# Kernel tuning notes

Hardware: AMD Instinct MI355X
Metric: run time of the kernel (lower is better)

## Reference

```python
import jax, jax.numpy as jnp
import numpy as np

N_NODES = 50000
N_EDGES = 800000
F_IN = 256
HID = 128
HEADS = 4
F_OUT = 64
NEG_SLOPE = 0.2


def setup_inputs() -> dict:
    key = jax.random.key(0)
    ks = jax.random.split(key, 12)
    x = jax.random.normal(ks[0], (N_NODES, F_IN), dtype=jnp.float32)
    edge_index = jax.random.randint(ks[1], (2, N_EDGES), 0, N_NODES, dtype=jnp.int64)
    s = 0.05
    return {
        "x": x,
        "edge_index": edge_index,
        "W1": jax.random.normal(ks[2], (F_IN, HEADS * HID), dtype=jnp.float32) * s,
        "a_src1": jax.random.normal(ks[3], (HEADS, HID), dtype=jnp.float32) * s,
        "a_dst1": jax.random.normal(ks[4], (HEADS, HID), dtype=jnp.float32) * s,
        "b1": jnp.zeros((HEADS * HID,), dtype=jnp.float32),
        "W2": jax.random.normal(ks[5], (HEADS * HID, F_OUT), dtype=jnp.float32) * s,
        "a_src2": jax.random.normal(ks[6], (1, F_OUT), dtype=jnp.float32) * s,
        "a_dst2": jax.random.normal(ks[7], (1, F_OUT), dtype=jnp.float32) * s,
        "b2": jnp.zeros((F_OUT,), dtype=jnp.float32),
    }


def _add_self_loops(edge_index, n):
    loop = jnp.arange(n, dtype=edge_index.dtype)
    return jnp.concatenate([edge_index, jnp.stack([loop, loop])], axis=1)


def _gat_conv(x, edge_index, W, a_src, a_dst, bias, heads, out_ch):
    # PyG GATConv: h = x @ W reshaped to [N, H, C]
    n = x.shape[0]
    h = (x @ W).reshape(n, heads, out_ch)
    # per-node attention logits [N, H]
    al_src = jnp.einsum('nhc,hc->nh', h, a_src)
    al_dst = jnp.einsum('nhc,hc->nh', h, a_dst)
    src, dst = edge_index[0], edge_index[1]
    e = jax.nn.leaky_relu(al_src[src] + al_dst[dst], NEG_SLOPE)  # [E, H]
    # softmax over incoming edges per destination node (segment softmax)
    e_max = jax.ops.segment_max(e, dst, num_segments=n)
    e_exp = jnp.exp(e - e_max[dst])
    denom = jax.ops.segment_sum(e_exp, dst, num_segments=n)
    alpha = e_exp / (denom[dst] + 1e-16)  # [E, H]
    msg = h[src] * alpha[:, :, None]  # [E, H, C]
    out = jax.ops.segment_sum(msg, dst, num_segments=n)  # [N, H, C]
    return out.reshape(n, heads * out_ch) + bias


def reference(x, edge_index, W1, a_src1, a_dst1, b1, W2, a_src2, a_dst2, b2):
    # Dropout layers are identity in eval mode.
    ei = _add_self_loops(edge_index, x.shape[0])
    h = jax.nn.elu(_gat_conv(x, ei, W1, a_src1, a_dst1, b1, HEADS, HID))
    out = _gat_conv(h, ei, W2, a_src2, a_dst2, b2, 1, F_OUT)
    return out
```

## Files before the change

### kernel.cpp

```cpp
#include <hip/hip_runtime.h>
#include <math.h>

#define N_NODES 50000
#define N_EDGES 800000
#define E_TOT   850000
#define F_IN    256
#define F1      512
#define HID     128
#define HEADS   4
#define F_OUT   64

typedef __attribute__((ext_vector_type(8))) short short8;
typedef __attribute__((ext_vector_type(4))) float f32x4;
typedef unsigned short ushort_t;
typedef unsigned int uint_t;

__device__ __forceinline__ float lrelu(float x){ return x > 0.f ? x : 0.2f*x; }
__device__ __forceinline__ float elu(float x){ return x > 0.f ? x : expm1f(x); }

__device__ __forceinline__ ushort_t f2b(float f){
  uint_t u = __builtin_bit_cast(uint_t, f);
  u += 0x7fffu + ((u >> 16) & 1u);
  return (ushort_t)(u >> 16);
}
__device__ __forceinline__ float blo(uint_t u){ return __builtin_bit_cast(float, u << 16); }
__device__ __forceinline__ float bhi(uint_t u){ return __builtin_bit_cast(float, u & 0xffff0000u); }
__device__ __forceinline__ float b2f(ushort_t s){ return __builtin_bit_cast(float, (uint_t)s << 16); }

__global__ void hist_kernel(const int* __restrict__ ei, int* __restrict__ deg){
  int e = blockIdx.x*blockDim.x + threadIdx.x;
  if (e >= E_TOT) return;
  int dst = (e < N_EDGES) ? ei[N_EDGES + e] : (e - N_EDGES);
  atomicAdd(&deg[dst], 1);
}

__global__ __launch_bounds__(256) void scan1_kernel(const int* __restrict__ deg,
                                                    int* __restrict__ offs,
                                                    int* __restrict__ bsum){
  __shared__ int sd[256];
  const int tid = threadIdx.x;
  const int i = blockIdx.x*256 + tid;
  int v = (i < N_NODES) ? deg[i] : 0;
  sd[tid] = v; __syncthreads();
  #pragma unroll
  for (int off = 1; off < 256; off <<= 1){
    int t = (tid >= off) ? sd[tid - off] : 0;
    __syncthreads();
    sd[tid] += t;
    __syncthreads();
  }
  if (i < N_NODES) offs[i] = sd[tid] - v;
  if (tid == 255) bsum[blockIdx.x] = sd[255];
}

__global__ __launch_bounds__(256) void scan2_kernel(const int* __restrict__ bsum,
                                                    int* __restrict__ bbase, int nb){
  __shared__ int sd[256];
  const int tid = threadIdx.x;
  int v = (tid < nb) ? bsum[tid] : 0;
  sd[tid] = v; __syncthreads();
  #pragma unroll
  for (int off = 1; off < 256; off <<= 1){
    int t = (tid >= off) ? sd[tid - off] : 0;
    __syncthreads();
    sd[tid] += t;
    __syncthreads();
  }
  if (tid < nb) bbase[tid] = sd[tid] - v;
}

__global__ __launch_bounds__(256) void scan3_kernel(int* __restrict__ offs,
                                                    const int* __restrict__ bbase,
                                                    int* __restrict__ cur){
  const int i = blockIdx.x*256 + threadIdx.x;
  if (i < N_NODES){
    int o = offs[i] + bbase[blockIdx.x];
    offs[i] = o;
    cur[i] = o;
  }
  if (blockIdx.x == 0 && threadIdx.x == 0) offs[N_NODES] = E_TOT;
}

__global__ void scatter_kernel(const int* __restrict__ ei, int* __restrict__ cur,
                               int* __restrict__ ssrc){
  int e = blockIdx.x*blockDim.x + threadIdx.x;
  if (e >= E_TOT) return;
  int src, dst;
  if (e < N_EDGES){ src = ei[e]; dst = ei[N_EDGES + e]; }
  else            { src = e - N_EDGES; dst = src; }
  int pos = atomicAdd(&cur[dst], 1);
  ssrc[pos] = src;
}

__global__ __launch_bounds__(256) void cvt_x_kernel(const float* __restrict__ x,
                                                    ushort_t* __restrict__ xb){
  const int t = blockIdx.x*256 + threadIdx.x;
  const float4 a = ((const float4*)x)[t*2];
  const float4 b = ((const float4*)x)[t*2 + 1];
  uint4 o;
  o.x = (uint_t)f2b(a.x) | ((uint_t)f2b(a.y) << 16);
  o.y = (uint_t)f2b(a.z) | ((uint_t)f2b(a.w) << 16);
  o.z = (uint_t)f2b(b.x) | ((uint_t)f2b(b.y) << 16);
  o.w = (uint_t)f2b(b.z) | ((uint_t)f2b(b.w) << 16);
  ((uint4*)xb)[t] = o;
}

__global__ __launch_bounds__(256) void transpose_bf16_kernel(const float* __restrict__ W,
                                                             ushort_t* __restrict__ Wt,
                                                             int K, int N){
  __shared__ float tile[64][65];
  const int k0 = blockIdx.x*64, n0 = blockIdx.y*64;
  const int c = threadIdx.x & 63, r4 = threadIdx.x >> 6;
  for (int r = r4; r < 64; r += 4)
    tile[r][c] = W[(size_t)(k0 + r)*N + n0 + c];
  __syncthreads();
  for (int r = r4; r < 64; r += 4)
    Wt[(size_t)(n0 + r)*K + k0 + c] = f2b(tile[c][r]);
}

template<int K, int WR, int WC>
__global__ __launch_bounds__(256) void gemm_bf16(const ushort_t* __restrict__ A,
                                                 const ushort_t* __restrict__ Bt,
                                                 ushort_t* __restrict__ C,
                                                 int M, int N){
  constexpr int BM = WR*64, BN = WC*64, BKP = 40;
  __shared__ ushort_t As[BM*BKP];
  __shared__ ushort_t Bs[BN*BKP];
  const int tid = threadIdx.x;
  const int wave = tid >> 6, lane = tid & 63, quad = lane >> 4, l16 = lane & 15;
  const int wm = wave % WR, wn = wave / WR;
  const int m0 = blockIdx.x*BM, n0 = blockIdx.y*BN;
  f32x4 acc[4][4] = {};
  for (int k0 = 0; k0 < K; k0 += 32){
    #pragma unroll
    for (int s = tid; s < BM*4; s += 256){
      int r = s >> 2, c = s & 3;
      int gr = m0 + r; if (gr >= M) gr = M - 1;
      *(uint4*)(As + r*BKP + c*8) = *(const uint4*)(A + (size_t)gr*K + k0 + c*8);
    }
    #pragma unroll
    for (int s = tid; s < BN*4; s += 256){
      int r = s >> 2, c = s & 3;
      *(uint4*)(Bs + r*BKP + c*8) = *(const uint4*)(Bt + (size_t)(n0 + r)*K + k0 + c*8);
    }
    __syncthreads();
    short8 af[4], bfr[4];
    #pragma unroll
    for (int i = 0; i < 4; ++i)
      af[i] = *(const short8*)(As + (wm*64 + i*16 + l16)*BKP + quad*8);
    #pragma unroll
    for (int j = 0; j < 4; ++j)
      bfr[j] = *(const short8*)(Bs + (wn*64 + j*16 + l16)*BKP + quad*8);
    #pragma unroll
    for (int i = 0; i < 4; ++i)
      #pragma unroll
      for (int j = 0; j < 4; ++j)
        acc[i][j] = __builtin_amdgcn_mfma_f32_16x16x32_bf16(af[i], bfr[j], acc[i][j], 0, 0, 0);
    __syncthreads();
  }
  #pragma unroll
  for (int i = 0; i < 4; ++i){
    #pragma unroll
    for (int r = 0; r < 4; ++r){
      int row = m0 + wm*64 + i*16 + quad*4 + r;
      if (row < M){
        #pragma unroll
        for (int j = 0; j < 4; ++j){
          int col = n0 + wn*64 + j*16 + l16;
          C[(size_t)row*N + col] = f2b(acc[i][j][r]);
        }
      }
    }
  }
}

__global__ __launch_bounds__(128) void logits1_kernel(const ushort_t* __restrict__ h1b,
                                                      const float* __restrict__ a_src,
                                                      const float* __restrict__ a_dst,
                                                      float* __restrict__ als,
                                                      float* __restrict__ ald){
  const int n = blockIdx.x;
  const int tid = threadIdx.x;
  const int head = tid >> 5, p = tid & 31;
  const uint2 v = *(const uint2*)(h1b + (size_t)n*F1 + tid*4);
  float h0 = blo(v.x), h1 = bhi(v.x), h2 = blo(v.y), h3 = bhi(v.y);
  const float4 as = *(const float4*)(a_src + head*HID + p*4);
  const float4 ad = *(const float4*)(a_dst + head*HID + p*4);
  float ds = h0*as.x + h1*as.y + h2*as.z + h3*as.w;
  float dd = h0*ad.x + h1*ad.y + h2*ad.z + h3*ad.w;
  #pragma unroll
  for (int off = 16; off >= 1; off >>= 1){
    ds += __shfl_down(ds, off, 32);
    dd += __shfl_down(dd, off, 32);
  }
  if (p == 0){ als[n*4 + head] = ds; ald[n*4 + head] = dd; }
}

__global__ __launch_bounds__(256) void agg1_kernel(const ushort_t* __restrict__ h1b,
                                                   const float* __restrict__ als,
                                                   const float* __restrict__ ald1,
                                                   const float* __restrict__ b1,
                                                   const int* __restrict__ offs,
                                                   const int* __restrict__ ssrc,
                                                   ushort_t* __restrict__ hb){
  __shared__ int   shsrc[4][64];
  __shared__ float shal[4][64][4];
  const int wave = threadIdx.x >> 6, lane = threadIdx.x & 63;
  const int n = blockIdx.x*4 + wave;
  const int head = lane >> 4;
  const float4 ald = ((const float4*)ald1)[n];
  const int s0 = offs[n], s1 = offs[n+1];

  float d0 = 0.f, d1 = 0.f, d2 = 0.f, d3 = 0.f;
  for (int e = s0 + lane; e < s1; e += 64){
    const int sc = ssrc[e];
    const float4 as = ((const float4*)als)[sc];
    d0 += __expf(lrelu(as.x + ald.x));
    d1 += __expf(lrelu(as.y + ald.y));
    d2 += __expf(lrelu(as.z + ald.z));
    d3 += __expf(lrelu(as.w + ald.w));
  }
  #pragma unroll
  for (int off = 32; off >= 1; off >>= 1){
    d0 += __shfl_xor(d0, off);
    d1 += __shfl_xor(d1, off);
    d2 += __shfl_xor(d2, off);
    d3 += __shfl_xor(d3, off);
  }
  const float den = (head == 0) ? d0 : (head == 1) ? d1 : (head == 2) ? d2 : d3;
  const float rd = 1.0f / (den + 1e-16f);

  float acc[8] = {0.f,0.f,0.f,0.f,0.f,0.f,0.f,0.f};
  for (int ce = s0; ce < s1; ce += 64){
    const int idx = ce + lane;
    if (idx < s1){
      const int sc = ssrc[idx];
      const float4 as = ((const float4*)als)[sc];
      shsrc[wave][lane] = sc;
      float4 a4;
      a4.x = __expf(lrelu(as.x + ald.x));
      a4.y = __expf(lrelu(as.y + ald.y));
      a4.z = __expf(lrelu(as.z + ald.z));
      a4.w = __expf(lrelu(as.w + ald.w));
      *(float4*)&shal[wave][lane][0] = a4;
    }
    const int nE = min(64, s1 - ce);
    for (int k = 0; k < nE; ++k){
      const int scb = shsrc[wave][k];
      const float al = shal[wave][k][head] * rd;
      const uint4 hv = *(const uint4*)(h1b + (size_t)scb*F1 + lane*8);
      acc[0] = fmaf(blo(hv.x), al, acc[0]);
      acc[1] = fmaf(bhi(hv.x), al, acc[1]);
      acc[2] = fmaf(blo(hv.y), al, acc[2]);
      acc[3] = fmaf(bhi(hv.y), al, acc[3]);
      acc[4] = fmaf(blo(hv.z), al, acc[4]);
      acc[5] = fmaf(bhi(hv.z), al, acc[5]);
      acc[6] = fmaf(blo(hv.w), al, acc[6]);
      acc[7] = fmaf(bhi(hv.w), al, acc[7]);
    }
  }
  const float4 ba = *(const float4*)(b1 + lane*8);
  const float4 bb = *(const float4*)(b1 + lane*8 + 4);
  float o0 = elu(acc[0] + ba.x), o1 = elu(acc[1] + ba.y);
  float o2 = elu(acc[2] + ba.z), o3 = elu(acc[3] + ba.w);
  float o4 = elu(acc[4] + bb.x), o5 = elu(acc[5] + bb.y);
  float o6 = elu(acc[6] + bb.z), o7 = elu(acc[7] + bb.w);
  uint4 o;
  o.x = (uint_t)f2b(o0) | ((uint_t)f2b(o1) << 16);
  o.y = (uint_t)f2b(o2) | ((uint_t)f2b(o3) << 16);
  o.z = (uint_t)f2b(o4) | ((uint_t)f2b(o5) << 16);
  o.w = (uint_t)f2b(o6) | ((uint_t)f2b(o7) << 16);
  *(uint4*)(hb + (size_t)n*F1 + lane*8) = o;
}

__global__ __launch_bounds__(64) void logits2_kernel(const ushort_t* __restrict__ gb,
                                                     const float* __restrict__ a_src,
                                                     const float* __restrict__ a_dst,
                                                     float* __restrict__ als,
                                                     float* __restrict__ ald){
  const int n = blockIdx.x;
  const int tid = threadIdx.x;
  const float v = b2f(gb[(size_t)n*F_OUT + tid]);
  float ds = v * a_src[tid];
  float dd = v * a_dst[tid];
  #pragma unroll
  for (int off = 32; off >= 1; off >>= 1){
    ds += __shfl_xor(ds, off);
    dd += __shfl_xor(dd, off);
  }
  if (tid == 0){ als[n] = ds; ald[n] = dd; }
}

__global__ __launch_bounds__(256) void agg2_kernel(const ushort_t* __restrict__ gb,
                                                   const float* __restrict__ als,
                                                   const float* __restrict__ ald2,
                                                   const float* __restrict__ b2,
                                                   const int* __restrict__ offs,
                                                   const int* __restrict__ ssrc,
                                                   float* __restrict__ out){
  __shared__ int   shsrc[4][64];
  __shared__ float shal[4][64];
  const int wave = threadIdx.x >> 6, lane = threadIdx.x & 63;
  const int n = blockIdx.x*4 + wave;
  const float ald = ald2[n];
  const int s0 = offs[n], s1 = offs[n+1];

  float dsum = 0.f;
  for (int e = s0 + lane; e < s1; e += 64)
    dsum += __expf(lrelu(als[ssrc[e]] + ald));
  #pragma unroll
  for (int off = 32; off >= 1; off >>= 1)
    dsum += __shfl_xor(dsum, off);
  const float rd = 1.0f / (dsum + 1e-16f);

  float acc = 0.f;
  for (int ce = s0; ce < s1; ce += 64){
    const int idx = ce + lane;
    if (idx < s1){
      const int sc = ssrc[idx];
      shsrc[wave][lane] = sc;
      shal[wave][lane] = __expf(lrelu(als[sc] + ald)) * rd;
    }
    const int nE = min(64, s1 - ce);
    for (int k = 0; k < nE; ++k){
      const int scb = shsrc[wave][k];
      const float al = shal[wave][k];
      acc = fmaf(b2f(gb[(size_t)scb*F_OUT + lane]), al, acc);
    }
  }
  out[(size_t)n*F_OUT + lane] = acc + b2[lane];
}

extern "C" void kernel_launch(void* const* d_in, const int* in_sizes, int n_in,
                              void* d_out, int out_size, void* d_ws, size_t ws_size,
                              hipStream_t stream){
  const float* x      = (const float*)d_in[0];
  const int*   ei     = (const int*)  d_in[1];
  const float* W1     = (const float*)d_in[2];
  const float* a_src1 = (const float*)d_in[3];
  const float* a_dst1 = (const float*)d_in[4];
  const float* b1     = (const float*)d_in[5];
  const float* W2     = (const float*)d_in[6];
  const float* a_src2 = (const float*)d_in[7];
  const float* a_dst2 = (const float*)d_in[8];
  const float* b2     = (const float*)d_in[9];
  float* out = (float*)d_out;

  char* ws = (char*)d_ws;
  ushort_t* h1b  = (ushort_t*)(ws + 0UL);
  ushort_t* hb   = (ushort_t*)(ws + 51200000UL);
  ushort_t* xb   = (ushort_t*)(ws + 102400000UL);
  ushort_t* gb   = (ushort_t*)(ws + 128000000UL);
  ushort_t* W1t  = (ushort_t*)(ws + 134400000UL);
  ushort_t* W2t  = (ushort_t*)(ws + 134662144UL);
  float*    als1 = (float*)   (ws + 134727680UL);
  float*    ald1 = (float*)   (ws + 135527680UL);
  float*    als2 = (float*)   (ws + 136327680UL);
  float*    ald2 = (float*)   (ws + 136527680UL);
  int*      deg  = (int*)     (ws + 136727680UL);
  int*      offs = (int*)     (ws + 136927680UL);
  int*      bsum = (int*)     (ws + 137127744UL);
  int*      bbase= (int*)     (ws + 137128544UL);
  int*      cur  = (int*)     (ws + 137129600UL);
  int*      ssrc = (int*)     (ws + 137329600UL);

  hipMemsetAsync(deg, 0, 200000, stream);

  const int eb = (E_TOT + 255) / 256;
  const int nb = (N_NODES + 255) / 256;
  hist_kernel   <<<eb, 256, 0, stream>>>(ei, deg);
  scan1_kernel  <<<nb, 256, 0, stream>>>(deg, offs, bsum);
  scan2_kernel  <<<1, 256, 0, stream>>>(bsum, bbase, nb);
  scan3_kernel  <<<nb, 256, 0, stream>>>(offs, bbase, cur);
  scatter_kernel<<<eb, 256, 0, stream>>>(ei, cur, ssrc);

  cvt_x_kernel        <<<6250, 256, 0, stream>>>(x, xb);
  transpose_bf16_kernel<<<dim3(4, 8), 256, 0, stream>>>(W1, W1t, F_IN, F1);
  transpose_bf16_kernel<<<dim3(8, 1), 256, 0, stream>>>(W2, W2t, F1, F_OUT);

  gemm_bf16<F_IN, 2, 2><<<dim3(391, 4), 256, 0, stream>>>(xb, W1t, h1b, N_NODES, F1);
  logits1_kernel<<<N_NODES, 128, 0, stream>>>(h1b, a_src1, a_dst1, als1, ald1);
  agg1_kernel   <<<12500, 256, 0, stream>>>(h1b, als1, ald1, b1, offs, ssrc, hb);

  gemm_bf16<F1, 4, 1><<<dim3(196, 1), 256, 0, stream>>>(hb, W2t, gb, N_NODES, F_OUT);
  logits2_kernel<<<N_NODES, 64, 0, stream>>>(gb, a_src2, a_dst2, als2, ald2);
  agg2_kernel   <<<12500, 256, 0, stream>>>(gb, als2, ald2, b2, offs, ssrc, out);
}
```

Baseline: 469.2 us.

## Use split-bf16 GEMMs with fused logits, sorted CSR, and vectorized layer-2 aggregation

Replaces the single-bf16 GEMMs with a three-MFMA hi/lo split scheme for higher accuracy. Attention logits are now computed in the GEMM epilogue, which removes the two separate logits kernels. The change also adds a per-node sort of source indices, loads GEMM tiles with global_load_lds, pre-normalizes alphas in agg1, stores layer-2 features as fp32 and vectorizes agg2 so each load fetches four edges. The split precision triples the MFMA work and doubles operand traffic, and the new sort kernel adds work of its own.

```diff
diff --git a/kernel.cpp b/kernel.cpp
--- a/kernel.cpp
+++ b/kernel.cpp
@@ -26,6 +26,16 @@
 __device__ __forceinline__ float blo(uint_t u){ return __builtin_bit_cast(float, u << 16); }
 __device__ __forceinline__ float bhi(uint_t u){ return __builtin_bit_cast(float, u & 0xffff0000u); }
 __device__ __forceinline__ float b2f(ushort_t s){ return __builtin_bit_cast(float, (uint_t)s << 16); }
+
+__device__ __forceinline__ void fsplit(float v, ushort_t& hi, ushort_t& lo){
+  hi = f2b(v);
+  lo = f2b(v - b2f(hi));
+}
+
+__device__ __forceinline__ void gld_lds16(const void* g, void* l){
+  __builtin_amdgcn_global_load_lds((const __attribute__((address_space(1))) unsigned int*)g,
+                                   (__attribute__((address_space(3))) unsigned int*)l, 16, 0, 0);
+}
 
 __global__ void hist_kernel(const int* __restrict__ ei, int* __restrict__ deg){
   int e = blockIdx.x*blockDim.x + threadIdx.x;
@@ -92,70 +102,127 @@
   ssrc[pos] = src;
 }
 
-__global__ __launch_bounds__(256) void cvt_x_kernel(const float* __restrict__ x,
-                                                    ushort_t* __restrict__ xb){
+__global__ __launch_bounds__(256) void sort_kernel(const int* __restrict__ offs,
+                                                   int* __restrict__ ssrc){
+  const int wave = threadIdx.x >> 6, lane = threadIdx.x & 63;
+  const int n = blockIdx.x*4 + wave;
+  const int s0 = offs[n];
+  const int len = offs[n+1] - s0;
+  if (len <= 1) return;
+  if (len <= 64){
+    int v = (lane < len) ? ssrc[s0 + lane] : 0x7fffffff;
+    for (int p = 0; p < len; ++p){
+      const int left = ((lane & 1) == (p & 1));
+      const int partner = left ? lane + 1 : lane - 1;
+      const int pv = __shfl(v, partner & 63);
+      const int nv = left ? min(v, pv) : max(v, pv);
+      v = (partner >= 0 && partner < 64) ? nv : v;
+    }
+    if (lane < len) ssrc[s0 + lane] = v;
+  } else if (lane == 0){
+    for (int i = 1; i < len; ++i){
+      int v = ssrc[s0 + i]; int j = i - 1;
+      while (j >= 0 && ssrc[s0 + j] > v){ ssrc[s0 + j + 1] = ssrc[s0 + j]; --j; }
+      ssrc[s0 + j + 1] = v;
+    }
+  }
+}
+
+__global__ __launch_bounds__(256) void cvt_x_split_kernel(const float* __restrict__ x,
+                                                          ushort_t* __restrict__ xh,
+                                                          ushort_t* __restrict__ xl){
   const int t = blockIdx.x*256 + threadIdx.x;
   const float4 a = ((const float4*)x)[t*2];
   const float4 b = ((const float4*)x)[t*2 + 1];
-  uint4 o;
-  o.x = (uint_t)f2b(a.x) | ((uint_t)f2b(a.y) << 16);
-  o.y = (uint_t)f2b(a.z) | ((uint_t)f2b(a.w) << 16);
-  o.z = (uint_t)f2b(b.x) | ((uint_t)f2b(b.y) << 16);
-  o.w = (uint_t)f2b(b.z) | ((uint_t)f2b(b.w) << 16);
-  ((uint4*)xb)[t] = o;
-}
-
-__global__ __launch_bounds__(256) void transpose_bf16_kernel(const float* __restrict__ W,
-                                                             ushort_t* __restrict__ Wt,
-                                                             int K, int N){
+  float v[8] = {a.x,a.y,a.z,a.w,b.x,b.y,b.z,b.w};
+  ushort_t h[8], l[8];
+  #pragma unroll
+  for (int i = 0; i < 8; ++i) fsplit(v[i], h[i], l[i]);
+  uint4 oh, ol;
+  oh.x = (uint_t)h[0] | ((uint_t)h[1] << 16);
+  oh.y = (uint_t)h[2] | ((uint_t)h[3] << 16);
+  oh.z = (uint_t)h[4] | ((uint_t)h[5] << 16);
+  oh.w = (uint_t)h[6] | ((uint_t)h[7] << 16);
+  ol.x = (uint_t)l[0] | ((uint_t)l[1] << 16);
+  ol.y = (uint_t)l[2] | ((uint_t)l[3] << 16);
+  ol.z = (uint_t)l[4] | ((uint_t)l[5] << 16);
+  ol.w = (uint_t)l[6] | ((uint_t)l[7] << 16);
+  ((uint4*)xh)[t] = oh;
+  ((uint4*)xl)[t] = ol;
+}
+
+__global__ __launch_bounds__(256) void transpose_split_kernel(const float* __restrict__ W,
+                                                              ushort_t* __restrict__ Wth,
+                                                              ushort_t* __restrict__ Wtl,
+                                                              int K, int N){
   __shared__ float tile[64][65];
   const int k0 = blockIdx.x*64, n0 = blockIdx.y*64;
   const int c = threadIdx.x & 63, r4 = threadIdx.x >> 6;
   for (int r = r4; r < 64; r += 4)
     tile[r][c] = W[(size_t)(k0 + r)*N + n0 + c];
   __syncthreads();
-  for (int r = r4; r < 64; r += 4)
-    Wt[(size_t)(n0 + r)*K + k0 + c] = f2b(tile[c][r]);
-}
-
-template<int K, int WR, int WC>
-__global__ __launch_bounds__(256) void gemm_bf16(const ushort_t* __restrict__ A,
-                                                 const ushort_t* __restrict__ Bt,
-                                                 ushort_t* __restrict__ C,
-                                                 int M, int N){
-  constexpr int BM = WR*64, BN = WC*64, BKP = 40;
-  __shared__ ushort_t As[BM*BKP];
-  __shared__ ushort_t Bs[BN*BKP];
+  for (int r = r4; r < 64; r += 4){
+    ushort_t hi, lo;
+    fsplit(tile[c][r], hi, lo);
+    Wth[(size_t)(n0 + r)*K + k0 + c] = hi;
+    Wtl[(size_t)(n0 + r)*K + k0 + c] = lo;
+  }
+}
+
+template<int K, int BM, int BN, int WR, int WC, int NH, int CH, bool CF32>
+__global__ __launch_bounds__(256) void gemm_x3(const ushort_t* __restrict__ Ah,
+                                               const ushort_t* __restrict__ Al,
+                                               const ushort_t* __restrict__ Bh,
+                                               const ushort_t* __restrict__ Bl,
+                                               void* __restrict__ Cout,
+                                               const float* __restrict__ a_src,
+                                               const float* __restrict__ a_dst,
+                                               float* __restrict__ als,
+                                               float* __restrict__ ald,
+                                               int M){
+  constexpr int NTOT = NH*CH;
+  __shared__ ushort_t Ash[BM*32], Asl[BM*32];
+  __shared__ ushort_t Bsh[BN*32], Bsl[BN*32];
+  __shared__ float slog[WC][BM][2];
   const int tid = threadIdx.x;
   const int wave = tid >> 6, lane = tid & 63, quad = lane >> 4, l16 = lane & 15;
   const int wm = wave % WR, wn = wave / WR;
-  const int m0 = blockIdx.x*BM, n0 = blockIdx.y*BN;
+  const int m0 = blockIdx.x*BM;
+  const int head = blockIdx.y;
+  const int n0 = head*BN;
   f32x4 acc[4][4] = {};
   for (int k0 = 0; k0 < K; k0 += 32){
+    for (int idx = tid; idx < BM*4; idx += 256){
+      int row = idx >> 2, ch = idx & 3;
+      int gr = m0 + row; gr = (gr < M) ? gr : (M - 1);
+      gld_lds16(Ah + (size_t)gr*K + k0 + ch*8, (char*)Ash + idx*16);
+      gld_lds16(Al + (size_t)gr*K + k0 + ch*8, (char*)Asl + idx*16);
+    }
+    for (int idx = tid; idx < BN*4; idx += 256){
+      int row = idx >> 2, ch = idx & 3;
+      gld_lds16(Bh + (size_t)(n0 + row)*K + k0 + ch*8, (char*)Bsh + idx*16);
+      gld_lds16(Bl + (size_t)(n0 + row)*K + k0 + ch*8, (char*)Bsl + idx*16);
+    }
+    __syncthreads();
+    short8 afh[4], afl[4], bfh[4], bfl[4];
     #pragma unroll
-    for (int s = tid; s < BM*4; s += 256){
-      int r = s >> 2, c = s & 3;
-      int gr = m0 + r; if (gr >= M) gr = M - 1;
-      *(uint4*)(As + r*BKP + c*8) = *(const uint4*)(A + (size_t)gr*K + k0 + c*8);
+    for (int i = 0; i < 4; ++i){
+      afh[i] = *(const short8*)(Ash + (wm*64 + i*16 + l16)*32 + quad*8);
+      afl[i] = *(const short8*)(Asl + (wm*64 + i*16 + l16)*32 + quad*8);
     }
     #pragma unroll
-    for (int s = tid; s < BN*4; s += 256){
-      int r = s >> 2, c = s & 3;
-      *(uint4*)(Bs + r*BKP + c*8) = *(const uint4*)(Bt + (size_t)(n0 + r)*K + k0 + c*8);
-    }
-    __syncthreads();
-    short8 af[4], bfr[4];
-    #pragma unroll
-    for (int i = 0; i < 4; ++i)
-      af[i] = *(const short8*)(As + (wm*64 + i*16 + l16)*BKP + quad*8);
-    #pragma unroll
-    for (int j = 0; j < 4; ++j)
-      bfr[j] = *(const short8*)(Bs + (wn*64 + j*16 + l16)*BKP + quad*8);
+    for (int j = 0; j < 4; ++j){
+      bfh[j] = *(const short8*)(Bsh + (wn*64 + j*16 + l16)*32 + quad*8);
+      bfl[j] = *(const short8*)(Bsl + (wn*64 + j*16 + l16)*32 + quad*8);
+    }
     #pragma unroll
     for (int i = 0; i < 4; ++i)
       #pragma unroll
-      for (int j = 0; j < 4; ++j)
-        acc[i][j] = __builtin_amdgcn_mfma_f32_16x16x32_bf16(af[i], bfr[j], acc[i][j], 0, 0, 0);
+      for (int j = 0; j < 4; ++j){
+        acc[i][j] = __builtin_amdgcn_mfma_f32_16x16x32_bf16(afh[i], bfh[j], acc[i][j], 0, 0, 0);
+        acc[i][j] = __builtin_amdgcn_mfma_f32_16x16x32_bf16(afl[i], bfh[j], acc[i][j], 0, 0, 0);
+        acc[i][j] = __builtin_amdgcn_mfma_f32_16x16x32_bf16(afh[i], bfl[j], acc[i][j], 0, 0, 0);
+      }
     __syncthreads();
   }
   #pragma unroll
@@ -167,33 +234,48 @@
         #pragma unroll
         for (int j = 0; j < 4; ++j){
           int col = n0 + wn*64 + j*16 + l16;
-          C[(size_t)row*N + col] = f2b(acc[i][j][r]);
+          if (CF32) ((float*)Cout)[(size_t)row*NTOT + col] = acc[i][j][r];
+          else      ((ushort_t*)Cout)[(size_t)row*NTOT + col] = f2b(acc[i][j][r]);
         }
       }
     }
   }
-}
-
-__global__ __launch_bounds__(128) void logits1_kernel(const ushort_t* __restrict__ h1b,
-                                                      const float* __restrict__ a_src,
-                                                      const float* __restrict__ a_dst,
-                                                      float* __restrict__ als,
-                                                      float* __restrict__ ald){
-  const int n = blockIdx.x;
-  const int tid = threadIdx.x;
-  const int head = tid >> 5, p = tid & 31;
-  const uint2 v = *(const uint2*)(h1b + (size_t)n*F1 + tid*4);
-  float h0 = blo(v.x), h1 = bhi(v.x), h2 = blo(v.y), h3 = bhi(v.y);
-  const float4 as = *(const float4*)(a_src + head*HID + p*4);
-  const float4 ad = *(const float4*)(a_dst + head*HID + p*4);
-  float ds = h0*as.x + h1*as.y + h2*as.z + h3*as.w;
-  float dd = h0*ad.x + h1*ad.y + h2*ad.z + h3*ad.w;
-  #pragma unroll
-  for (int off = 16; off >= 1; off >>= 1){
-    ds += __shfl_down(ds, off, 32);
-    dd += __shfl_down(dd, off, 32);
-  }
-  if (p == 0){ als[n*4 + head] = ds; ald[n*4 + head] = dd; }
+  float aws[4], awd[4];
+  #pragma unroll
+  for (int j = 0; j < 4; ++j){
+    int cih = wn*64 + j*16 + l16;
+    aws[j] = a_src[head*CH + cih];
+    awd[j] = a_dst[head*CH + cih];
+  }
+  #pragma unroll
+  for (int i = 0; i < 4; ++i){
+    #pragma unroll
+    for (int r = 0; r < 4; ++r){
+      float s = acc[i][0][r]*aws[0] + acc[i][1][r]*aws[1]
+              + acc[i][2][r]*aws[2] + acc[i][3][r]*aws[3];
+      float d = acc[i][0][r]*awd[0] + acc[i][1][r]*awd[1]
+              + acc[i][2][r]*awd[2] + acc[i][3][r]*awd[3];
+      #pragma unroll
+      for (int off = 8; off >= 1; off >>= 1){
+        s += __shfl_xor(s, off);
+        d += __shfl_xor(d, off);
+      }
+      if (l16 == 0){
+        slog[wn][wm*64 + i*16 + quad*4 + r][0] = s;
+        slog[wn][wm*64 + i*16 + quad*4 + r][1] = d;
+      }
+    }
+  }
+  __syncthreads();
+  for (int t = tid; t < BM; t += 256){
+    float s = slog[0][t][0], d = slog[0][t][1];
+    if (WC > 1){ s += slog[WC-1][t][0]; d += slog[WC-1][t][1]; }
+    int row = m0 + t;
+    if (row < M){
+      als[row*NH + head] = s;
+      ald[row*NH + head] = d;
+    }
+  }
 }
 
 __global__ __launch_bounds__(256) void agg1_kernel(const ushort_t* __restrict__ h1b,
@@ -202,7 +284,8 @@
                                                    const float* __restrict__ b1,
                                                    const int* __restrict__ offs,
                                                    const int* __restrict__ ssrc,
-                                                   ushort_t* __restrict__ hb){
+                                                   ushort_t* __restrict__ hbh,
+                                                   ushort_t* __restrict__ hbl){
   __shared__ int   shsrc[4][64];
   __shared__ float shal[4][64][4];
   const int wave = threadIdx.x >> 6, lane = threadIdx.x & 63;
@@ -227,8 +310,8 @@
     d2 += __shfl_xor(d2, off);
     d3 += __shfl_xor(d3, off);
   }
-  const float den = (head == 0) ? d0 : (head == 1) ? d1 : (head == 2) ? d2 : d3;
-  const float rd = 1.0f / (den + 1e-16f);
+  const float rd0 = 1.0f/(d0 + 1e-16f), rd1 = 1.0f/(d1 + 1e-16f);
+  const float rd2 = 1.0f/(d2 + 1e-16f), rd3 = 1.0f/(d3 + 1e-16f);
 
   float acc[8] = {0.f,0.f,0.f,0.f,0.f,0.f,0.f,0.f};
   for (int ce = s0; ce < s1; ce += 64){
@@ -238,60 +321,53 @@
       const float4 as = ((const float4*)als)[sc];
       shsrc[wave][lane] = sc;
       float4 a4;
-      a4.x = __expf(lrelu(as.x + ald.x));
-      a4.y = __expf(lrelu(as.y + ald.y));
-      a4.z = __expf(lrelu(as.z + ald.z));
-      a4.w = __expf(lrelu(as.w + ald.w));
+      a4.x = __expf(lrelu(as.x + ald.x)) * rd0;
+      a4.y = __expf(lrelu(as.y + ald.y)) * rd1;
+      a4.z = __expf(lrelu(as.z + ald.z)) * rd2;
+      a4.w = __expf(lrelu(as.w + ald.w)) * rd3;
       *(float4*)&shal[wave][lane][0] = a4;
     }
+    __builtin_amdgcn_wave_barrier();
     const int nE = min(64, s1 - ce);
     for (int k = 0; k < nE; ++k){
-      const int scb = shsrc[wave][k];
-      const float al = shal[wave][k][head] * rd;
-      const uint4 hv = *(const uint4*)(h1b + (size_t)scb*F1 + lane*8);
-      acc[0] = fmaf(blo(hv.x), al, acc[0]);
-      acc[1] = fmaf(bhi(hv.x), al, acc[1]);
-      acc[2] = fmaf(blo(hv.y), al, acc[2]);
-      acc[3] = fmaf(bhi(hv.y), al, acc[3]);
-      acc[4] = fmaf(blo(hv.z), al, acc[4]);
-      acc[5] = fmaf(bhi(hv.z), al, acc[5]);
-      acc[6] = fmaf(blo(hv.w), al, acc[6]);
-      acc[7] = fmaf(bhi(hv.w), al, acc[7]);
-    }
+      const int sa = shsrc[wave][k];
+      const float aa = shal[wave][k][head];
+      const uint4 ha = *(const uint4*)(h1b + (size_t)sa*F1 + lane*8);
+      acc[0] = fmaf(blo(ha.x), aa, acc[0]);
+      acc[1] = fmaf(bhi(ha.x), aa, acc[1]);
+      acc[2] = fmaf(blo(ha.y), aa, acc[2]);
+      acc[3] = fmaf(bhi(ha.y), aa, acc[3]);
+      acc[4] = fmaf(blo(ha.z), aa, acc[4]);
+      acc[5] = fmaf(bhi(ha.z), aa, acc[5]);
+      acc[6] = fmaf(blo(ha.w), aa, acc[6]);
+      acc[7] = fmaf(bhi(ha.w), aa, acc[7]);
+    }
+    __builtin_amdgcn_wave_barrier();
   }
   const float4 ba = *(const float4*)(b1 + lane*8);
   const float4 bb = *(const float4*)(b1 + lane*8 + 4);
-  float o0 = elu(acc[0] + ba.x), o1 = elu(acc[1] + ba.y);
-  float o2 = elu(acc[2] + ba.z), o3 = elu(acc[3] + ba.w);
-  float o4 = elu(acc[4] + bb.x), o5 = elu(acc[5] + bb.y);
-  float o6 = elu(acc[6] + bb.z), o7 = elu(acc[7] + bb.w);
-  uint4 o;
-  o.x = (uint_t)f2b(o0) | ((uint_t)f2b(o1) << 16);
-  o.y = (uint_t)f2b(o2) | ((uint_t)f2b(o3) << 16);
-  o.z = (uint_t)f2b(o4) | ((uint_t)f2b(o5) << 16);
-  o.w = (uint_t)f2b(o6) | ((uint_t)f2b(o7) << 16);
-  *(uint4*)(hb + (size_t)n*F1 + lane*8) = o;
-}
-
-__global__ __launch_bounds__(64) void logits2_kernel(const ushort_t* __restrict__ gb,
-                                                     const float* __restrict__ a_src,
-                                                     const float* __restrict__ a_dst,
-                                                     float* __restrict__ als,
-                                                     float* __restrict__ ald){
-  const int n = blockIdx.x;
-  const int tid = threadIdx.x;
-  const float v = b2f(gb[(size_t)n*F_OUT + tid]);
-  float ds = v * a_src[tid];
-  float dd = v * a_dst[tid];
-  #pragma unroll
-  for (int off = 32; off >= 1; off >>= 1){
-    ds += __shfl_xor(ds, off);
-    dd += __shfl_xor(dd, off);
-  }
-  if (tid == 0){ als[n] = ds; ald[n] = dd; }
-}
-
-__global__ __launch_bounds__(256) void agg2_kernel(const ushort_t* __restrict__ gb,
+  float o[8];
+  o[0] = elu(acc[0] + ba.x); o[1] = elu(acc[1] + ba.y);
+  o[2] = elu(acc[2] + ba.z); o[3] = elu(acc[3] + ba.w);
+  o[4] = elu(acc[4] + bb.x); o[5] = elu(acc[5] + bb.y);
+  o[6] = elu(acc[6] + bb.z); o[7] = elu(acc[7] + bb.w);
+  ushort_t h[8], l[8];
+  #pragma unroll
+  for (int i = 0; i < 8; ++i) fsplit(o[i], h[i], l[i]);
+  uint4 oh, ol;
+  oh.x = (uint_t)h[0] | ((uint_t)h[1] << 16);
+  oh.y = (uint_t)h[2] | ((uint_t)h[3] << 16);
+  oh.z = (uint_t)h[4] | ((uint_t)h[5] << 16);
+  oh.w = (uint_t)h[6] | ((uint_t)h[7] << 16);
+  ol.x = (uint_t)l[0] | ((uint_t)l[1] << 16);
+  ol.y = (uint_t)l[2] | ((uint_t)l[3] << 16);
+  ol.z = (uint_t)l[4] | ((uint_t)l[5] << 16);
+  ol.w = (uint_t)l[6] | ((uint_t)l[7] << 16);
+  *(uint4*)(hbh + (size_t)n*F1 + lane*8) = oh;
+  *(uint4*)(hbl + (size_t)n*F1 + lane*8) = ol;
+}
+
+__global__ __launch_bounds__(256) void agg2_kernel(const float* __restrict__ gb,
                                                    const float* __restrict__ als,
                                                    const float* __restrict__ ald2,
                                                    const float* __restrict__ b2,
@@ -302,6 +378,7 @@
   __shared__ float shal[4][64];
   const int wave = threadIdx.x >> 6, lane = threadIdx.x & 63;
   const int n = blockIdx.x*4 + wave;
+  const int g = lane >> 4, l16 = lane & 15;
   const float ald = ald2[n];
   const int s0 = offs[n], s1 = offs[n+1];
 
@@ -313,7 +390,7 @@
     dsum += __shfl_xor(dsum, off);
   const float rd = 1.0f / (dsum + 1e-16f);
 
-  float acc = 0.f;
+  float a0 = 0.f, a1 = 0.f, a2 = 0.f, a3 = 0.f;
   for (int ce = s0; ce < s1; ce += 64){
     const int idx = ce + lane;
     if (idx < s1){
@@ -321,14 +398,30 @@
       shsrc[wave][lane] = sc;
       shal[wave][lane] = __expf(lrelu(als[sc] + ald)) * rd;
     }
+    __builtin_amdgcn_wave_barrier();
     const int nE = min(64, s1 - ce);
-    for (int k = 0; k < nE; ++k){
-      const int scb = shsrc[wave][k];
-      const float al = shal[wave][k];
-      acc = fmaf(b2f(gb[(size_t)scb*F_OUT + lane]), al, acc);
-    }
-  }
-  out[(size_t)n*F_OUT + lane] = acc + b2[lane];
+    for (int k = 0; k < nE; k += 4){
+      const int e = k + g;
+      float al = 0.f;
+      int sc = shsrc[wave][0];
+      if (e < nE){ sc = shsrc[wave][e]; al = shal[wave][e]; }
+      const float4 hv = *(const float4*)(gb + (size_t)sc*F_OUT + l16*4);
+      a0 = fmaf(hv.x, al, a0);
+      a1 = fmaf(hv.y, al, a1);
+      a2 = fmaf(hv.z, al, a2);
+      a3 = fmaf(hv.w, al, a3);
+    }
+    __builtin_amdgcn_wave_barrier();
+  }
+  a0 += __shfl_xor(a0, 16); a0 += __shfl_xor(a0, 32);
+  a1 += __shfl_xor(a1, 16); a1 += __shfl_xor(a1, 32);
+  a2 += __shfl_xor(a2, 16); a2 += __shfl_xor(a2, 32);
+  a3 += __shfl_xor(a3, 16); a3 += __shfl_xor(a3, 32);
+  if (g == 0){
+    const float4 bv = *(const float4*)(b2 + l16*4);
+    float4 o = {a0 + bv.x, a1 + bv.y, a2 + bv.z, a3 + bv.w};
+    *(float4*)(out + (size_t)n*F_OUT + l16*4) = o;
+  }
 }
 
 extern "C" void kernel_launch(void* const* d_in, const int* in_sizes, int n_in,
@@ -347,22 +440,26 @@
   float* out = (float*)d_out;
 
   char* ws = (char*)d_ws;
-  ushort_t* h1b  = (ushort_t*)(ws + 0UL);
-  ushort_t* hb   = (ushort_t*)(ws + 51200000UL);
-  ushort_t* xb   = (ushort_t*)(ws + 102400000UL);
-  ushort_t* gb   = (ushort_t*)(ws + 128000000UL);
-  ushort_t* W1t  = (ushort_t*)(ws + 134400000UL);
-  ushort_t* W2t  = (ushort_t*)(ws + 134662144UL);
-  float*    als1 = (float*)   (ws + 134727680UL);
-  float*    ald1 = (float*)   (ws + 135527680UL);
-  float*    als2 = (float*)   (ws + 136327680UL);
-  float*    ald2 = (float*)   (ws + 136527680UL);
-  int*      deg  = (int*)     (ws + 136727680UL);
-  int*      offs = (int*)     (ws + 136927680UL);
-  int*      bsum = (int*)     (ws + 137127744UL);
-  int*      bbase= (int*)     (ws + 137128544UL);
-  int*      cur  = (int*)     (ws + 137129600UL);
-  int*      ssrc = (int*)     (ws + 137329600UL);
+  ushort_t* xh   = (ushort_t*)(ws + 0UL);
+  ushort_t* xl   = (ushort_t*)(ws + 25600000UL);
+  ushort_t* hbh  = (ushort_t*)(ws + 0UL);
+  ushort_t* h1b  = (ushort_t*)(ws + 51200000UL);
+  ushort_t* hbl  = (ushort_t*)(ws + 102400000UL);
+  float*    gb   = (float*)   (ws + 153600000UL);
+  ushort_t* W1th = (ushort_t*)(ws + 166400000UL);
+  ushort_t* W1tl = (ushort_t*)(ws + 166662144UL);
+  ushort_t* W2th = (ushort_t*)(ws + 166924288UL);
+  ushort_t* W2tl = (ushort_t*)(ws + 166989824UL);
+  float*    als1 = (float*)   (ws + 167055360UL);
+  float*    ald1 = (float*)   (ws + 167855360UL);
+  float*    als2 = (float*)   (ws + 168655360UL);
+  float*    ald2 = (float*)   (ws + 168855360UL);
+  int*      deg  = (int*)     (ws + 169055360UL);
+  int*      offs = (int*)     (ws + 169255360UL);
+  int*      bsum = (int*)     (ws + 169455616UL);
+  int*      bbase= (int*)     (ws + 169456640UL);
+  int*      cur  = (int*)     (ws + 169457664UL);
+  int*      ssrc = (int*)     (ws + 169657664UL);
 
   hipMemsetAsync(deg, 0, 200000, stream);
 
@@ -373,16 +470,19 @@
   scan2_kernel  <<<1, 256, 0, stream>>>(bsum, bbase, nb);
   scan3_kernel  <<<nb, 256, 0, stream>>>(offs, bbase, cur);
   scatter_kernel<<<eb, 256, 0, stream>>>(ei, cur, ssrc);
-
-  cvt_x_kernel        <<<6250, 256, 0, stream>>>(x, xb);
-  transpose_bf16_kernel<<<dim3(4, 8), 256, 0, stream>>>(W1, W1t, F_IN, F1);
-  transpose_bf16_kernel<<<dim3(8, 1), 256, 0, stream>>>(W2, W2t, F1, F_OUT);
-
-  gemm_bf16<F_IN, 2, 2><<<dim3(391, 4), 256, 0, stream>>>(xb, W1t, h1b, N_NODES, F1);
-  logits1_kernel<<<N_NODES, 128, 0, stream>>>(h1b, a_src1, a_dst1, als1, ald1);
-  agg1_kernel   <<<12500, 256, 0, stream>>>(h1b, als1, ald1, b1, offs, ssrc, hb);
-
-  gemm_bf16<F1, 4, 1><<<dim3(196, 1), 256, 0, stream>>>(hb, W2t, gb, N_NODES, F_OUT);
-  logits2_kernel<<<N_NODES, 64, 0, stream>>>(gb, a_src2, a_dst2, als2, ald2);
-  agg2_kernel   <<<12500, 256, 0, stream>>>(gb, als2, ald2, b2, offs, ssrc, out);
-}
+  sort_kernel   <<<12500, 256, 0, stream>>>(offs, ssrc);
+
+  cvt_x_split_kernel   <<<6250, 256, 0, stream>>>(x, xh, xl);
+  transpose_split_kernel<<<dim3(4, 8), 256, 0, stream>>>(W1, W1th, W1tl, F_IN, F1);
+  transpose_split_kernel<<<dim3(8, 1), 256, 0, stream>>>(W2, W2th, W2tl, F1, F_OUT);
+
+  gemm_x3<F_IN, 128, 128, 2, 2, 4, 128, false>
+    <<<dim3(391, 4), 256, 0, stream>>>(xh, xl, W1th, W1tl, h1b,
+                                       a_src1, a_dst1, als1, ald1, N_NODES);
+  agg1_kernel<<<12500, 256, 0, stream>>>(h1b, als1, ald1, b1, offs, ssrc, hbh, hbl);
+
+  gemm_x3<F1, 256, 64, 4, 1, 1, 64, true>
+    <<<dim3(196, 1), 256, 0, stream>>>(hbh, hbl, W2th, W2tl, gb,
+                                       a_src2, a_dst2, als2, ald2, N_NODES);
+  agg2_kernel<<<12500, 256, 0, stream>>>(gb, als2, ald2, b2, offs, ssrc, out);
+}
```

Result: slower. 521.4 us (+11.1%).
